# Performance work log

Measured on AMD Instinct MI355X. Metric: run time of the kernel, lower is better.

Reference implementation:

```python
import jax, jax.numpy as jnp
import numpy as np

N_NODES = 100000
N_EDGES = 1600000
IN_F = 128
OUT_F = 64


def setup_inputs() -> dict:
    key = jax.random.key(0)
    ks = jax.random.split(key, 9)
    x = jax.random.normal(ks[0], (N_NODES, IN_F), dtype=jnp.float32)
    Wv = jax.random.normal(ks[1], (IN_F, OUT_F), dtype=jnp.float32) / np.sqrt(IN_F)
    bv = jax.random.normal(ks[2], (OUT_F,), dtype=jnp.float32) * 0.02
    wq = jax.random.normal(ks[3], (OUT_F,), dtype=jnp.float32) / np.sqrt(OUT_F)
    bq = jax.random.normal(ks[4], (1,), dtype=jnp.float32) * 0.02
    wk = jax.random.normal(ks[5], (OUT_F,), dtype=jnp.float32) / np.sqrt(OUT_F)
    bk = jax.random.normal(ks[6], (1,), dtype=jnp.float32) * 0.02
    src = jax.random.randint(ks[7], (N_EDGES,), 0, N_NODES, dtype=jnp.int64)
    dst = jax.random.randint(ks[8], (N_EDGES,), 0, N_NODES, dtype=jnp.int64)
    return {"x": x, "Wv": Wv, "bv": bv, "wq": wq, "bq": bq,
            "wk": wk, "bk": bk, "src": src, "dst": dst}


def reference(x, Wv, bv, wq, bq, wk, bk, src, dst):
    n = x.shape[0]
    # node transform (linear_v) and scalar scores (linear_q, linear_k)
    xv = x @ Wv + bv                      # [N, OUT_F]
    el = xv @ wq + bq[0]                  # [N] source score
    er = xv @ wk + bk[0]                  # [N] destination score
    # per-edge score: u_add_v + leaky_relu(0.2)
    e = jax.nn.leaky_relu(el[src] + er[dst], negative_slope=0.2)  # [E]
    # edge softmax over incoming edges of each dst (numerically stable)
    emax = jax.ops.segment_max(e, dst, num_segments=n)            # [N]
    ex = jnp.exp(e - emax[dst])                                   # [E]
    denom = jax.ops.segment_sum(ex, dst, num_segments=n)          # [N]
    attn = ex / denom[dst]                                        # [E]
    # u_mul_e + aggregate_sum: weighted scatter of source features into dst
    out = jax.ops.segment_sum(xv[src] * attn[:, None], dst, num_segments=n)
    return out
```

## Files before the change

kernel.cpp:

```cpp
#include <hip/hip_runtime.h>
#include <hip/hip_bf16.h>

#define NN 100000
#define NE 1600000
#define IN_F 128
#define OUT_F 64
#define NBINS 782
#define BIN_SHIFT 7
#define GEMM_WGS 1563
#define P1_WGS 391
#define NREP2 8
#define SUBCAP 384
#define XS_STRIDE 136

typedef __attribute__((ext_vector_type(8))) short bf16x8;
typedef __attribute__((ext_vector_type(4))) float f32x4;

__device__ __forceinline__ short f2bf(float f) {
  unsigned u = __float_as_uint(f);
  unsigned r = (u + 0x7fffu + ((u >> 16) & 1u)) >> 16;
  return (short)r;
}
__device__ __forceinline__ float bf2f(ushort u) {
  return __uint_as_float(((unsigned)u) << 16);
}

__global__ __launch_bounds__(256) void prep_w(
    const float* __restrict__ Wv, short* __restrict__ wvt,
    int* __restrict__ bincur) {
  if (blockIdx.x == 0)
    for (int i = threadIdx.x; i < NREP2 * NBINS; i += 256) bincur[i] = 0;
  const int i = blockIdx.x * 256 + threadIdx.x;
  if (i >= IN_F * OUT_F) return;
  const int j = i >> 7, k = i & 127;
  wvt[i] = f2bf(Wv[k * OUT_F + j]);
}

__global__ __launch_bounds__(256) void fused_tp(
    const float* __restrict__ x, const short* __restrict__ wvt,
    const float* __restrict__ bv, const float* __restrict__ wq,
    const float* __restrict__ bq, const float* __restrict__ wk,
    const float* __restrict__ bk,
    ushort* __restrict__ xvb, float* __restrict__ el, float* __restrict__ er,
    const int* __restrict__ src, const int* __restrict__ dst,
    int* __restrict__ bincur, unsigned* __restrict__ slab) {
  __shared__ __align__(16) char smem_[19712];
  if (blockIdx.x < P1_WGS) {
    int* hist = (int*)smem_;
    int* base_ = hist + NBINS;
    const int pb = blockIdx.x;
    const int t = threadIdx.x;
    const int rep = pb & (NREP2 - 1);
    for (int i = t; i < NBINS; i += 256) hist[i] = 0;
    __syncthreads();
    const int e0 = pb * 4096;
    int sv[16], dv[16];
#pragma unroll
    for (int r = 0; r < 16; ++r) {
      const int i = e0 + r * 256 + t;
      if (i < NE) {
        sv[r] = src[i];
        dv[r] = dst[i];
        atomicAdd(&hist[dv[r] >> BIN_SHIFT], 1);
      } else {
        sv[r] = -1;
        dv[r] = 0;
      }
    }
    __syncthreads();
    for (int b = t; b < NBINS; b += 256) {
      base_[b] = (hist[b] > 0) ? atomicAdd(&bincur[rep * NBINS + b], hist[b]) : 0;
      hist[b] = 0;
    }
    __syncthreads();
#pragma unroll
    for (int r = 0; r < 16; ++r) {
      if (sv[r] >= 0) {
        const int s = sv[r], d = dv[r];
        const int b = d >> BIN_SHIFT;
        const unsigned dl = (unsigned)(d & 127);
        const int pos = base_[b] + atomicAdd(&hist[b], 1);
        slab[(size_t)(b * NREP2 + rep) * SUBCAP + pos] = (dl << 17) | (unsigned)s;
      }
    }
    return;
  }

  ushort* xs = (ushort*)smem_;
  float* pql = (float*)(smem_ + 64 * XS_STRIDE * 2);
  float* pkl = pql + 256;
  const int gb = blockIdx.x - P1_WGS;
  const int node0 = gb * 64;
  const int t = threadIdx.x;
  const int wave = t >> 6, lane = t & 63;
  const int j15 = lane & 15, g = lane >> 4;

#pragma unroll
  for (int i = 0; i < 8; ++i) {
    const int idx = i * 256 + t;
    const int row = idx >> 5, col4 = (idx & 31) << 2;
    int grow = node0 + row;
    if (grow >= NN) grow = NN - 1;
    const float4 v = *(const float4*)(x + (size_t)grow * IN_F + col4);
    ushort4 h;
    h.x = (ushort)f2bf(v.x); h.y = (ushort)f2bf(v.y);
    h.z = (ushort)f2bf(v.z); h.w = (ushort)f2bf(v.w);
    *(ushort4*)(xs + row * XS_STRIDE + col4) = h;
  }

  const int nt = wave;
  bf16x8 b[4];
#pragma unroll
  for (int kt = 0; kt < 4; ++kt)
    b[kt] = *(const bf16x8*)(wvt + (size_t)(nt * 16 + j15) * IN_F + kt * 32 + g * 8);

  const float bvl = bv[nt * 16 + j15];
  const float wql = wq[nt * 16 + j15];
  const float wkl = wk[nt * 16 + j15];
  const float bq0 = bq[0], bk0 = bk[0];

  __syncthreads();

#pragma unroll
  for (int ntile = 0; ntile < 4; ++ntile) {
    f32x4 acc = (f32x4){0.f, 0.f, 0.f, 0.f};
#pragma unroll
    for (int kt = 0; kt < 4; ++kt) {
      const bf16x8 a = *(const bf16x8*)(xs + (ntile * 16 + j15) * XS_STRIDE + kt * 32 + g * 8);
      acc = __builtin_amdgcn_mfma_f32_16x16x32_bf16(a, b[kt], acc, 0, 0, 0);
    }
#pragma unroll
    for (int r = 0; r < 4; ++r) {
      const int nl = ntile * 16 + g * 4 + r;
      const int node = node0 + nl;
      const float v = acc[r] + bvl;
      if (node < NN) xvb[(size_t)node * OUT_F + nt * 16 + j15] = (ushort)f2bf(v);
      float pq = v * wql, pk = v * wkl;
#pragma unroll
      for (int o = 1; o < 16; o <<= 1) {
        pq += __shfl_xor(pq, o);
        pk += __shfl_xor(pk, o);
      }
      if (j15 == 0) {
        pql[nl * 4 + nt] = pq;
        pkl[nl * 4 + nt] = pk;
      }
    }
  }
  __syncthreads();
  if (t < 64) {
    const int node = node0 + t;
    if (node < NN) {
      el[node] = pql[t * 4] + pql[t * 4 + 1] + pql[t * 4 + 2] + pql[t * 4 + 3] + bq0;
      er[node] = pkl[t * 4] + pkl[t * 4 + 1] + pkl[t * 4 + 2] + pkl[t * 4 + 3] + bk0;
    }
  }
}

__global__ __launch_bounds__(256) void bin_scatter(
    const unsigned* __restrict__ slab, const int* __restrict__ bincur,
    const float* __restrict__ el, const float* __restrict__ er,
    int* __restrict__ off, uint2* __restrict__ csr) {
  __shared__ int sp[256];
  __shared__ int cnt[128];
  __shared__ float er_l[128];
  __shared__ int s_csr0;
  const int b = blockIdx.x, t = threadIdx.x;
  const int n0 = b << BIN_SHIFT;

  int v = 0;
#pragma unroll
  for (int j = 0; j < 4; ++j) {
    const int bb = 4 * t + j;
    if (bb < NBINS) {
#pragma unroll
      for (int r = 0; r < NREP2; ++r) v += bincur[r * NBINS + bb];
    }
  }
  sp[t] = v;
  __syncthreads();
  for (int o = 1; o < 256; o <<= 1) {
    const int u = (t >= o) ? sp[t - o] : 0;
    __syncthreads();
    sp[t] += u;
    __syncthreads();
  }
  if (t == 0) {
    const int q = b >> 2, rr = b & 3;
    int c = (q > 0) ? sp[q - 1] : 0;
    for (int j = 0; j < rr; ++j)
      for (int r = 0; r < NREP2; ++r) c += bincur[r * NBINS + (4 * q + j)];
    s_csr0 = c;
  }
  if (t < 128) {
    cnt[t] = 0;
    const int n = n0 + t;
    er_l[t] = (n < NN) ? er[n] : 0.f;
  }
  __syncthreads();
  const int csr0 = s_csr0;

#pragma unroll
  for (int rep = 0; rep < NREP2; ++rep) {
    const int c = bincur[rep * NBINS + b];
    const unsigned* sl = slab + (size_t)(b * NREP2 + rep) * SUBCAP;
    for (int i = t; i < c; i += 256)
      atomicAdd(&cnt[sl[i] >> 17], 1);
  }
  __syncthreads();

  const int cme = (t < 128) ? cnt[t] : 0;
  sp[t] = cme;
  __syncthreads();
  for (int o = 1; o < 128; o <<= 1) {
    const int u = (t >= o && t < 128) ? sp[t - o] : 0;
    __syncthreads();
    if (t < 128) sp[t] += u;
    __syncthreads();
  }
  if (t < 128) {
    const int cur = csr0 + sp[t] - cme;
    cnt[t] = cur;
    if (n0 + t < NN) off[n0 + t] = cur;
  }
  if (b == NBINS - 1 && t == 0) off[NN] = NE;
  __syncthreads();

#pragma unroll
  for (int rep = 0; rep < NREP2; ++rep) {
    const int c = bincur[rep * NBINS + b];
    const unsigned* sl = slab + (size_t)(b * NREP2 + rep) * SUBCAP;
    for (int i = t; i < c; i += 256) {
      const unsigned w = sl[i];
      const int dl = (int)(w >> 17);
      const int s = (int)(w & 0x1FFFFu);
      float e = el[s] + er_l[dl];
      e = e > 0.f ? e : 0.2f * e;
      const int pos = atomicAdd(&cnt[dl], 1);
      csr[pos] = (uint2){(unsigned)s, __float_as_uint(e)};
    }
  }
}

__global__ __launch_bounds__(256) void node_aggregate(
    const ushort* __restrict__ xvb, const int* __restrict__ off,
    const uint2* __restrict__ csr, float* __restrict__ out) {
  const int wave = threadIdx.x >> 6, lane = threadIdx.x & 63;
  const int node = blockIdx.x * 4 + wave;
  if (node >= NN) return;
  const int base = off[node];
  const int deg = off[node + 1] - base;

  if (deg <= 64) {
    const bool valid = lane < deg;
    uint2 w = valid ? csr[base + lane] : (uint2){0u, 0u};
    int s = (int)w.x;
    float p = valid ? __expf(__uint_as_float(w.y)) : 0.f;
    float t = p;
#pragma unroll
    for (int o = 32; o; o >>= 1) t += __shfl_xor(t, o);
    p *= (deg > 0) ? (1.0f / t) : 0.f;

    const int fgrp = lane & 7, egrp = lane >> 3;
    float4 aLo = {0.f, 0.f, 0.f, 0.f};
    float4 aHi = {0.f, 0.f, 0.f, 0.f};
    const int nr = (deg + 7) >> 3;
#pragma unroll 4
    for (int r = 0; r < nr; ++r) {
      const int k = (r << 3) + egrp;
      const int sk = __shfl(s, k);
      const float pk = __shfl(p, k);
      if (k < deg) {
        const uint4 v = *(const uint4*)(xvb + (size_t)sk * OUT_F + (fgrp << 3));
        aLo.x += pk * __uint_as_float(v.x << 16);
        aLo.y += pk * __uint_as_float(v.x & 0xffff0000u);
        aLo.z += pk * __uint_as_float(v.y << 16);
        aLo.w += pk * __uint_as_float(v.y & 0xffff0000u);
        aHi.x += pk * __uint_as_float(v.z << 16);
        aHi.y += pk * __uint_as_float(v.z & 0xffff0000u);
        aHi.z += pk * __uint_as_float(v.w << 16);
        aHi.w += pk * __uint_as_float(v.w & 0xffff0000u);
      }
    }
#pragma unroll
    for (int o = 8; o <= 32; o <<= 1) {
      aLo.x += __shfl_xor(aLo.x, o);
      aLo.y += __shfl_xor(aLo.y, o);
      aLo.z += __shfl_xor(aLo.z, o);
      aLo.w += __shfl_xor(aLo.w, o);
      aHi.x += __shfl_xor(aHi.x, o);
      aHi.y += __shfl_xor(aHi.y, o);
      aHi.z += __shfl_xor(aHi.z, o);
      aHi.w += __shfl_xor(aHi.w, o);
    }
    if (egrp == 0) {
      float* op = out + (size_t)node * OUT_F + (fgrp << 3);
      *(float4*)op = aLo;
      *(float4*)(op + 4) = aHi;
    }
  } else {
    float m = -3.0e38f;
    for (int k = lane; k < deg; k += 64) m = fmaxf(m, __uint_as_float(csr[base + k].y));
#pragma unroll
    for (int o = 32; o; o >>= 1) m = fmaxf(m, __shfl_xor(m, o));
    float ssum = 0.f;
    for (int k = lane; k < deg; k += 64) ssum += __expf(__uint_as_float(csr[base + k].y) - m);
#pragma unroll
    for (int o = 32; o; o >>= 1) ssum += __shfl_xor(ssum, o);
    const float inv = 1.0f / ssum;
    float acc = 0.f;
    for (int k = 0; k < deg; ++k) {
      const uint2 w = csr[base + k];
      const float pk = __expf(__uint_as_float(w.y) - m) * inv;
      acc += pk * bf2f(xvb[(size_t)w.x * OUT_F + lane]);
    }
    out[(size_t)node * OUT_F + lane] = acc;
  }
}

extern "C" void kernel_launch(void* const* d_in, const int* in_sizes, int n_in,
                              void* d_out, int out_size, void* d_ws, size_t ws_size,
                              hipStream_t stream) {
  const float* x  = (const float*)d_in[0];
  const float* Wv = (const float*)d_in[1];
  const float* bv = (const float*)d_in[2];
  const float* wq = (const float*)d_in[3];
  const float* bq = (const float*)d_in[4];
  const float* wk = (const float*)d_in[5];
  const float* bk = (const float*)d_in[6];
  const int* src  = (const int*)d_in[7];
  const int* dst  = (const int*)d_in[8];
  float* out = (float*)d_out;

  ushort* xvb = (ushort*)d_ws;
  float* el = (float*)(xvb + (size_t)NN * OUT_F);
  float* er = el + NN;
  int* off = (int*)(er + NN);
  uint2* csr = (uint2*)(off + NN + 2);
  unsigned* slab = (unsigned*)(csr + NE);
  short* wvt = (short*)(slab + (size_t)NBINS * NREP2 * SUBCAP);
  int* bincur = (int*)(wvt + IN_F * OUT_F);

  prep_w<<<(IN_F * OUT_F + 255) / 256, 256, 0, stream>>>(Wv, wvt, bincur);
  fused_tp<<<P1_WGS + GEMM_WGS, 256, 0, stream>>>(x, wvt, bv, wq, bq, wk, bk,
                                                  xvb, el, er, src, dst, bincur, slab);
  bin_scatter<<<NBINS, 256, 0, stream>>>(slab, bincur, el, er, off, csr);
  node_aggregate<<<(NN + 3) / 4, 256, 0, stream>>>(xvb, off, csr, out);
}
```

Measured before the change: 109.0 us.

## Drop prep_w kernel, convert Wv inline, split el/er into separate GEMV kernel

Removes the prep_w launch: the bincur zeroing becomes a hipMemsetAsync and the GEMM blocks now read fp32 Wv directly and convert it to bf16 in registers, using strided scalar loads. The el/er score reduction (shuffles plus an LDS pass) is moved out of the GEMM epilogue into a new gemv_eler kernel that re-reads the bf16 xv rows. This shortens the GEMM blocks and frees shared memory, but adds a kernel launch, an extra pass over xv, and computes el/er from bf16-rounded values rather than the fp32 accumulator.

Result: slower. 114.4 us (+5.0%).

```diff
diff --git a/kernel.cpp b/kernel.cpp
--- a/kernel.cpp
+++ b/kernel.cpp
@@ -25,26 +25,13 @@
   return __uint_as_float(((unsigned)u) << 16);
 }
 
-__global__ __launch_bounds__(256) void prep_w(
-    const float* __restrict__ Wv, short* __restrict__ wvt,
-    int* __restrict__ bincur) {
-  if (blockIdx.x == 0)
-    for (int i = threadIdx.x; i < NREP2 * NBINS; i += 256) bincur[i] = 0;
-  const int i = blockIdx.x * 256 + threadIdx.x;
-  if (i >= IN_F * OUT_F) return;
-  const int j = i >> 7, k = i & 127;
-  wvt[i] = f2bf(Wv[k * OUT_F + j]);
-}
-
 __global__ __launch_bounds__(256) void fused_tp(
-    const float* __restrict__ x, const short* __restrict__ wvt,
-    const float* __restrict__ bv, const float* __restrict__ wq,
-    const float* __restrict__ bq, const float* __restrict__ wk,
-    const float* __restrict__ bk,
-    ushort* __restrict__ xvb, float* __restrict__ el, float* __restrict__ er,
+    const float* __restrict__ x, const float* __restrict__ Wv,
+    const float* __restrict__ bv,
+    ushort* __restrict__ xvb,
     const int* __restrict__ src, const int* __restrict__ dst,
     int* __restrict__ bincur, unsigned* __restrict__ slab) {
-  __shared__ __align__(16) char smem_[19712];
+  __shared__ __align__(16) char smem_[17408];
   if (blockIdx.x < P1_WGS) {
     int* hist = (int*)smem_;
     int* base_ = hist + NBINS;
@@ -87,8 +74,6 @@
   }
 
   ushort* xs = (ushort*)smem_;
-  float* pql = (float*)(smem_ + 64 * XS_STRIDE * 2);
-  float* pkl = pql + 256;
   const int gb = blockIdx.x - P1_WGS;
   const int node0 = gb * 64;
   const int t = threadIdx.x;
@@ -109,15 +94,17 @@
   }
 
   const int nt = wave;
+  const int jcol = nt * 16 + j15;
   bf16x8 b[4];
 #pragma unroll
-  for (int kt = 0; kt < 4; ++kt)
-    b[kt] = *(const bf16x8*)(wvt + (size_t)(nt * 16 + j15) * IN_F + kt * 32 + g * 8);
-
-  const float bvl = bv[nt * 16 + j15];
-  const float wql = wq[nt * 16 + j15];
-  const float wkl = wk[nt * 16 + j15];
-  const float bq0 = bq[0], bk0 = bk[0];
+  for (int kt = 0; kt < 4; ++kt) {
+    const int k0 = kt * 32 + g * 8;
+    bf16x8 tb;
+#pragma unroll
+    for (int e = 0; e < 8; ++e) tb[e] = f2bf(Wv[(size_t)(k0 + e) * OUT_F + jcol]);
+    b[kt] = tb;
+  }
+  const float bvl = bv[jcol];
 
   __syncthreads();
 
@@ -131,30 +118,41 @@
     }
 #pragma unroll
     for (int r = 0; r < 4; ++r) {
-      const int nl = ntile * 16 + g * 4 + r;
-      const int node = node0 + nl;
-      const float v = acc[r] + bvl;
-      if (node < NN) xvb[(size_t)node * OUT_F + nt * 16 + j15] = (ushort)f2bf(v);
-      float pq = v * wql, pk = v * wkl;
-#pragma unroll
-      for (int o = 1; o < 16; o <<= 1) {
-        pq += __shfl_xor(pq, o);
-        pk += __shfl_xor(pk, o);
-      }
-      if (j15 == 0) {
-        pql[nl * 4 + nt] = pq;
-        pkl[nl * 4 + nt] = pk;
-      }
-    }
-  }
-  __syncthreads();
-  if (t < 64) {
-    const int node = node0 + t;
-    if (node < NN) {
-      el[node] = pql[t * 4] + pql[t * 4 + 1] + pql[t * 4 + 2] + pql[t * 4 + 3] + bq0;
-      er[node] = pkl[t * 4] + pkl[t * 4 + 1] + pkl[t * 4 + 2] + pkl[t * 4 + 3] + bk0;
-    }
-  }
+      const int node = node0 + ntile * 16 + g * 4 + r;
+      if (node < NN)
+        xvb[(size_t)node * OUT_F + jcol] = (ushort)f2bf(acc[r] + bvl);
+    }
+  }
+}
+
+__global__ __launch_bounds__(256) void gemv_eler(
+    const ushort* __restrict__ xvb, const float* __restrict__ wq,
+    const float* __restrict__ bq, const float* __restrict__ wk,
+    const float* __restrict__ bk,
+    float* __restrict__ el, float* __restrict__ er) {
+  __shared__ float swq[OUT_F], swk[OUT_F];
+  const int t = threadIdx.x;
+  if (t < OUT_F) { swq[t] = wq[t]; swk[t] = wk[t]; }
+  __syncthreads();
+  const int node = blockIdx.x * 256 + t;
+  if (node >= NN) return;
+  const ushort* xr = xvb + (size_t)node * OUT_F;
+  float pq = 0.f, pk = 0.f;
+#pragma unroll
+  for (int i = 0; i < 8; ++i) {
+    const uint4 v = *(const uint4*)(xr + i * 8);
+    const unsigned uu[4] = {v.x, v.y, v.z, v.w};
+#pragma unroll
+    for (int h = 0; h < 4; ++h) {
+      const float lo = __uint_as_float(uu[h] << 16);
+      const float hi = __uint_as_float(uu[h] & 0xffff0000u);
+      const int j = i * 8 + h * 2;
+      pq += lo * swq[j] + hi * swq[j + 1];
+      pk += lo * swk[j] + hi * swk[j + 1];
+    }
+  }
+  el[node] = pq + bq[0];
+  er[node] = pk + bk[0];
 }
 
 __global__ __launch_bounds__(256) void bin_scatter(
@@ -338,12 +336,13 @@
   int* off = (int*)(er + NN);
   uint2* csr = (uint2*)(off + NN + 2);
   unsigned* slab = (unsigned*)(csr + NE);
-  short* wvt = (short*)(slab + (size_t)NBINS * NREP2 * SUBCAP);
-  int* bincur = (int*)(wvt + IN_F * OUT_F);
-
-  prep_w<<<(IN_F * OUT_F + 255) / 256, 256, 0, stream>>>(Wv, wvt, bincur);
-  fused_tp<<<P1_WGS + GEMM_WGS, 256, 0, stream>>>(x, wvt, bv, wq, bq, wk, bk,
-                                                  xvb, el, er, src, dst, bincur, slab);
+  int* bincur = (int*)(slab + (size_t)NBINS * NREP2 * SUBCAP);
+
+  hipMemsetAsync(bincur, 0, NREP2 * NBINS * sizeof(int), stream);
+
+  fused_tp<<<P1_WGS + GEMM_WGS, 256, 0, stream>>>(x, Wv, bv, xvb, src, dst,
+                                                  bincur, slab);
+  gemv_eler<<<(NN + 255) / 256, 256, 0, stream>>>(xvb, wq, bq, wk, bk, el, er);
   bin_scatter<<<NBINS, 256, 0, stream>>>(slab, bincur, el, er, off, csr);
   node_aggregate<<<(NN + 3) / 4, 256, 0, stream>>>(xvb, off, csr, out);
 }
```
